# Kernel tuning notes

Measured on AMD Instinct MI355X. Metric: run time of the kernel, lower is better.

## Reference

```python
import jax, jax.numpy as jnp
import numpy as np

D_MODEL = 768
N_HEADS = 12
D_K = D_MODEL // N_HEADS


def setup_inputs() -> dict:
    key = jax.random.key(0)
    ks = jax.random.split(key, 9)
    s = 1.0 / np.sqrt(D_MODEL)
    return {
        "x": jax.random.normal(ks[0], (2, 2048, D_MODEL), dtype=jnp.float32),
        "w_q": jax.random.normal(ks[1], (D_MODEL, D_MODEL), dtype=jnp.float32) * s,
        "b_q": jax.random.normal(ks[2], (D_MODEL,), dtype=jnp.float32) * 0.02,
        "w_k": jax.random.normal(ks[3], (D_MODEL, D_MODEL), dtype=jnp.float32) * s,
        "b_k": jax.random.normal(ks[4], (D_MODEL,), dtype=jnp.float32) * 0.02,
        "w_v": jax.random.normal(ks[5], (D_MODEL, D_MODEL), dtype=jnp.float32) * s,
        "b_v": jax.random.normal(ks[6], (D_MODEL,), dtype=jnp.float32) * 0.02,
        "w_o": jax.random.normal(ks[7], (D_MODEL, D_MODEL), dtype=jnp.float32) * s,
        "b_o": jax.random.normal(ks[8], (D_MODEL,), dtype=jnp.float32) * 0.02,
    }


def reference(x, w_q, b_q, w_k, b_k, w_v, b_v, w_o, b_o):
    B, S, _ = x.shape
    # nn.Linear: y = x @ W^T + b
    def proj(w, b):
        y = jnp.einsum("bsd,ed->bse", x, w) + b
        # [B, S, D] -> [B, H, S, d_k]
        return y.reshape(B, S, N_HEADS, D_K).transpose(0, 2, 1, 3)

    q = proj(w_q, b_q)
    k = proj(w_k, b_k)
    v = proj(w_v, b_v)

    scale = 1.0 / np.sqrt(D_K).astype(np.float32)
    scores = jnp.einsum("bhqd,bhkd->bhqk", q, k) * scale  # [B,H,S,S]
    attn = jax.nn.softmax(scores, axis=-1)
    ctx = jnp.einsum("bhqk,bhkd->bhqd", attn, v)  # [B,H,S,d_k]
    ctx = ctx.transpose(0, 2, 1, 3).reshape(B, S, D_MODEL)
    out = jnp.einsum("bsd,ed->bse", ctx, w_o) + b_o
    return out
```

## Files before the change

### kernel.cpp

```cpp
#include <hip/hip_runtime.h>
#include <hip/hip_bf16.h>

#define B_   2
#define S_   2048
#define D_   768
#define H_   12
#define DK_  64
#define R_   (B_*S_)
#define LOG2E_OVER8 0.18033688011112042f

typedef __attribute__((ext_vector_type(8))) short short8;
typedef __attribute__((ext_vector_type(4))) float f32x4;

__device__ __forceinline__ short f2b(float f) {
  union { float f; unsigned u; } x; x.f = f;
  unsigned r = x.u + 0x7fffu + ((x.u >> 16) & 1u);
  return (short)(r >> 16);
}

__device__ __forceinline__ unsigned cvt_pk_bf16(float lo, float hi) {
  unsigned r;
  asm("v_cvt_pk_bf16_f32 %0, %1, %2" : "=v"(r) : "v"(lo), "v"(hi));
  return r;
}

__device__ __forceinline__ void gl_lds16(const short* g, short* l) {
  __builtin_amdgcn_global_load_lds(
      (const __attribute__((address_space(1))) void*)g,
      (__attribute__((address_space(3))) void*)l, 16, 0, 0);
}

__global__ void cvt_kernel(const float* __restrict__ x,
                           const float* __restrict__ wq, const float* __restrict__ wk,
                           const float* __restrict__ wv, const float* __restrict__ wo,
                           short* __restrict__ xb, short* __restrict__ wb) {
  const int XQ = R_ * D_ / 4;
  const int WQ = D_ * D_ / 4;
  int idx = blockIdx.x * blockDim.x + threadIdx.x;
  const float* src; short* dst; int off;
  if (idx < XQ) { src = x; dst = xb; off = idx; }
  else {
    int wi = idx - XQ; int w = wi / WQ; off = wi - w * WQ;
    if      (w == 0) { src = wq; dst = wb; }
    else if (w == 1) { src = wk; dst = wb + D_*D_; }
    else if (w == 2) { src = wv; dst = wb + 2*D_*D_; }
    else             { src = wo; dst = wb + 3*D_*D_; }
  }
  float4 v = ((const float4*)src)[off];
  short4 o;
  o.x = f2b(v.x); o.y = f2b(v.y); o.z = f2b(v.z); o.w = f2b(v.w);
  ((short4*)dst)[off] = o;
}

__launch_bounds__(256)
__global__ void qkv_gemm_kernel(const short* __restrict__ xb, const short* __restrict__ wb,
                                const float* __restrict__ bq, const float* __restrict__ bk,
                                const float* __restrict__ bv,
                                short* __restrict__ Qw, short* __restrict__ Kw,
                                short* __restrict__ VTw) {
  __shared__ short As[2][128 * 32];
  __shared__ short Bs[2][128 * 32];
  const int which = blockIdx.z;
  const short* W = wb + which * (D_ * D_);
  const float* bias = (which == 0) ? bq : (which == 1) ? bk : bv;
  const int n0 = blockIdx.x * 128, m0 = blockIdx.y * 128;
  const int t = threadIdx.x, l = t & 63, w = t >> 6;
  const int wr = w >> 1, wc = w & 1;

  f32x4 acc[4][4] = {};
  const int srow = t >> 2, sseg = (t & 3) * 8;

#define GSTAGE(buf, k0) do { \
    gl_lds16(xb + (m0 + srow) * D_ + (k0) + sseg,      &As[buf][t * 8]); \
    gl_lds16(xb + (m0 + 64 + srow) * D_ + (k0) + sseg, &As[buf][(t + 256) * 8]); \
    gl_lds16(W  + (n0 + srow) * D_ + (k0) + sseg,      &Bs[buf][t * 8]); \
    gl_lds16(W  + (n0 + 64 + srow) * D_ + (k0) + sseg, &Bs[buf][(t + 256) * 8]); \
  } while (0)

  GSTAGE(0, 0);
  __syncthreads();
  int cur = 0;
  for (int k0 = 0; k0 < D_; k0 += 32) {
    if (k0 + 32 < D_) GSTAGE(cur ^ 1, k0 + 32);
    short8 a[4], b[4];
#pragma unroll
    for (int i = 0; i < 4; i++)
      a[i] = *(const short8*)&As[cur][(wr * 64 + i * 16 + (l & 15)) * 32 + (l >> 4) * 8];
#pragma unroll
    for (int i = 0; i < 4; i++)
      b[i] = *(const short8*)&Bs[cur][(wc * 64 + i * 16 + (l & 15)) * 32 + (l >> 4) * 8];
#pragma unroll
    for (int i = 0; i < 4; i++)
#pragma unroll
      for (int j = 0; j < 4; j++)
        acc[i][j] = __builtin_amdgcn_mfma_f32_16x16x32_bf16(a[i], b[j], acc[i][j], 0, 0, 0);
    __syncthreads();
    cur ^= 1;
  }
#undef GSTAGE

#pragma unroll
  for (int i = 0; i < 4; i++) {
#pragma unroll
    for (int j2 = 0; j2 < 4; j2++) {
      int mm = m0 + wr * 64 + i * 16 + (l >> 4) * 4 + j2;
      int bidx = mm >> 11, s = mm & 2047;
#pragma unroll
      for (int nj = 0; nj < 4; nj++) {
        int e = n0 + wc * 64 + nj * 16 + (l & 15);
        float val = acc[i][nj][j2] + bias[e];
        int h = e >> 6, dk = e & 63;
        int bh = bidx * H_ + h;
        if (which == 0)      Qw[(bh * S_ + s) * DK_ + dk] = f2b(val * LOG2E_OVER8);
        else if (which == 1) Kw[(bh * S_ + s) * DK_ + dk] = f2b(val);
        else                 VTw[(bh * DK_ + dk) * S_ + s] = f2b(val);
      }
    }
  }
}

#define KVB   32
#define SHALF 1024
__launch_bounds__(256, 3)
__global__ void attn_kernel(const short* __restrict__ Qw, const short* __restrict__ Kw,
                            const short* __restrict__ VTw, short* __restrict__ ctx) {
  __shared__ short Ksh[2][2][KVB * DK_];
  __shared__ short Vsh[2][2][KVB * DK_];

  const int t = threadIdx.x, l = t & 63, w = t >> 6;
  const int s = w >> 1, qh = w & 1;
  const int L = blockIdx.y * 32 + blockIdx.x;
  const int xcd = L & 7, idx = L >> 3;
  const int bh = xcd * 3 + (idx >> 5);
  const int qblk = idx & 31;
  const int q0 = qblk * 64 + qh * 32;
  const int bq = bh / H_, h = bh - bq * H_;
  const short* Qh = Qw + bh * S_ * DK_;
  const short* Kh = Kw + (bh * S_ + s * SHALF) * DK_;
  const short* Vh = VTw + bh * DK_ * S_ + s * SHALF;

  const int tt = t & 127;
  const int kr0 = tt >> 3, kc0 = tt & 7;
  const int koff0 = kr0 * DK_ + ((kc0 ^ (kr0 & 7)) << 3);
  const int vc8 = (tt & 7) ^ ((tt >> 3) & 7);
  const int vr0 = 2 * (tt >> 3) + (vc8 >> 2);
  const int voff0 = vr0 * S_ + ((vc8 & 3) << 3);

#define STAGE(buf, kt) do { \
    gl_lds16(Kh + (kt) * DK_ + koff0,        &Ksh[s][buf][tt * 8]); \
    gl_lds16(Kh + (kt) * DK_ + koff0 + 1024, &Ksh[s][buf][tt * 8 + 1024]); \
    gl_lds16(Vh + (kt) + voff0,              &Vsh[s][buf][tt * 8]); \
    gl_lds16(Vh + (kt) + voff0 + 32 * S_,    &Vsh[s][buf][tt * 8 + 1024]); \
  } while (0)

  short8 qf[2][2];
#pragma unroll
  for (int mi = 0; mi < 2; mi++)
#pragma unroll
    for (int ks = 0; ks < 2; ks++)
      qf[mi][ks] = *(const short8*)&Qh[(q0 + 16 * mi + (l & 15)) * DK_ + ks * 32 + (l >> 4) * 8];

  f32x4 acc_o[2][4] = {};
  float l_run[2] = {0.f, 0.f};

  STAGE(0, 0);
  __syncthreads();
  int cur = 0;

  for (int kt = 0; kt < SHALF; kt += KVB) {
    if (kt + KVB < SHALF) STAGE(cur ^ 1, kt + KVB);

    f32x4 acc_s[2][2] = {};
    __builtin_amdgcn_s_setprio(1);
#pragma unroll
    for (int ni = 0; ni < 2; ni++) {
      int r = (l & 15) + 16 * ni;
#pragma unroll
      for (int ks = 0; ks < 2; ks++) {
        int cc = (l >> 4) + 4 * ks;
        short8 kf = *(const short8*)&Ksh[s][cur][r * DK_ + ((cc ^ (r & 7)) << 3)];
        acc_s[0][ni] = __builtin_amdgcn_mfma_f32_16x16x32_bf16(kf, qf[0][ks], acc_s[0][ni], 0, 0, 0);
        acc_s[1][ni] = __builtin_amdgcn_mfma_f32_16x16x32_bf16(kf, qf[1][ks], acc_s[1][ni], 0, 0, 0);
      }
    }
    __builtin_amdgcn_s_setprio(0);

#pragma unroll
    for (int mi = 0; mi < 2; mi++) {
      float sum = 0.f;
#pragma unroll
      for (int ni = 0; ni < 2; ni++)
#pragma unroll
        for (int j = 0; j < 4; j++) {
          float p = __builtin_amdgcn_exp2f(acc_s[mi][ni][j]);
          acc_s[mi][ni][j] = p;
          sum += p;
        }
      l_run[mi] += sum;
    }

    union PK { unsigned u[4]; short8 v; } pa0, pa1;
    pa0.u[0] = cvt_pk_bf16(acc_s[0][0][0], acc_s[0][0][1]);
    pa0.u[1] = cvt_pk_bf16(acc_s[0][0][2], acc_s[0][0][3]);
    pa0.u[2] = cvt_pk_bf16(acc_s[0][1][0], acc_s[0][1][1]);
    pa0.u[3] = cvt_pk_bf16(acc_s[0][1][2], acc_s[0][1][3]);
    pa1.u[0] = cvt_pk_bf16(acc_s[1][0][0], acc_s[1][0][1]);
    pa1.u[1] = cvt_pk_bf16(acc_s[1][0][2], acc_s[1][0][3]);
    pa1.u[2] = cvt_pk_bf16(acc_s[1][1][0], acc_s[1][1][1]);
    pa1.u[3] = cvt_pk_bf16(acc_s[1][1][2], acc_s[1][1][3]);

    __builtin_amdgcn_s_setprio(1);
    {
      const int cc = l >> 4;
      union V8 { short4 h[2]; short8 v; };
#pragma unroll
      for (int nd = 0; nd < 4; nd++) {
        int vr = (l & 15) + 16 * nd, rp = vr >> 1;
        int ph0 = (((vr & 1) << 2) | (cc >> 1)) ^ (rp & 7);
        int ph1 = (((vr & 1) << 2) | (2 + (cc >> 1))) ^ (rp & 7);
        V8 vf;
        vf.h[0] = *(const short4*)&Vsh[s][cur][rp * 64 + ph0 * 8 + (cc & 1) * 4];
        vf.h[1] = *(const short4*)&Vsh[s][cur][rp * 64 + ph1 * 8 + (cc & 1) * 4];
        acc_o[0][nd] = __builtin_amdgcn_mfma_f32_16x16x32_bf16(pa0.v, vf.v, acc_o[0][nd], 0, 0, 0);
        acc_o[1][nd] = __builtin_amdgcn_mfma_f32_16x16x32_bf16(pa1.v, vf.v, acc_o[1][nd], 0, 0, 0);
      }
    }
    __builtin_amdgcn_s_setprio(0);

    __syncthreads();
    cur ^= 1;
  }

#pragma unroll
  for (int mi = 0; mi < 2; mi++) {
    l_run[mi] += __shfl_xor(l_run[mi], 16);
    l_run[mi] += __shfl_xor(l_run[mi], 32);
  }

  __syncthreads();
  float* Oshf = (float*)&Ksh[0][0][0];
  float* Lsh  = (float*)&Vsh[0][0][0];
  if (s == 1) {
#pragma unroll
    for (int mi = 0; mi < 2; mi++)
#pragma unroll
      for (int nd = 0; nd < 4; nd++)
#pragma unroll
        for (int j = 0; j < 4; j++)
          Oshf[qh * 2048 + (16 * mi + (l >> 4) * 4 + j) * 64 + (l & 15) + 16 * nd] = acc_o[mi][nd][j];
    if (l < 16) {
      Lsh[(qh * 2 + 0) * 16 + l] = l_run[0];
      Lsh[(qh * 2 + 1) * 16 + l] = l_run[1];
    }
  }
  __syncthreads();
  if (s == 0) {
#pragma unroll
    for (int mi = 0; mi < 2; mi++) {
#pragma unroll
      for (int j = 0; j < 4; j++) {
        int src = ((l >> 4) << 2) + j;
        float llo = __shfl(l_run[mi], src);
        float lhi = Lsh[(qh * 2 + mi) * 16 + src];
        float inv = 1.f / (llo + lhi);
        int srow = q0 + 16 * mi + src;
#pragma unroll
        for (int nd = 0; nd < 4; nd++) {
          float ohi = Oshf[qh * 2048 + (16 * mi + src) * 64 + (l & 15) + 16 * nd];
          float val = (acc_o[mi][nd][j] + ohi) * inv;
          ctx[(bq * S_ + srow) * D_ + h * DK_ + (l & 15) + 16 * nd] = f2b(val);
        }
      }
    }
  }
#undef STAGE
}

__launch_bounds__(256)
__global__ void oproj_kernel(const short* __restrict__ ctx, const short* __restrict__ Wo,
                             const float* __restrict__ bo, float* __restrict__ out) {
  __shared__ short As[2][128 * 32];
  __shared__ short Bs[2][128 * 32];
  const int n0 = blockIdx.x * 128, m0 = blockIdx.y * 128;
  const int t = threadIdx.x, l = t & 63, w = t >> 6;
  const int wr = w >> 1, wc = w & 1;

  f32x4 acc[4][4] = {};
  const int srow = t >> 2, sseg = (t & 3) * 8;

#define GSTAGE(buf, k0) do { \
    gl_lds16(ctx + (m0 + srow) * D_ + (k0) + sseg,      &As[buf][t * 8]); \
    gl_lds16(ctx + (m0 + 64 + srow) * D_ + (k0) + sseg, &As[buf][(t + 256) * 8]); \
    gl_lds16(Wo  + (n0 + srow) * D_ + (k0) + sseg,      &Bs[buf][t * 8]); \
    gl_lds16(Wo  + (n0 + 64 + srow) * D_ + (k0) + sseg, &Bs[buf][(t + 256) * 8]); \
  } while (0)

  GSTAGE(0, 0);
  __syncthreads();
  int cur = 0;
  for (int k0 = 0; k0 < D_; k0 += 32) {
    if (k0 + 32 < D_) GSTAGE(cur ^ 1, k0 + 32);
    short8 a[4], b[4];
#pragma unroll
    for (int i = 0; i < 4; i++)
      a[i] = *(const short8*)&As[cur][(wr * 64 + i * 16 + (l & 15)) * 32 + (l >> 4) * 8];
#pragma unroll
    for (int i = 0; i < 4; i++)
      b[i] = *(const short8*)&Bs[cur][(wc * 64 + i * 16 + (l & 15)) * 32 + (l >> 4) * 8];
#pragma unroll
    for (int i = 0; i < 4; i++)
#pragma unroll
      for (int j = 0; j < 4; j++)
        acc[i][j] = __builtin_amdgcn_mfma_f32_16x16x32_bf16(a[i], b[j], acc[i][j], 0, 0, 0);
    __syncthreads();
    cur ^= 1;
  }
#undef GSTAGE

#pragma unroll
  for (int i = 0; i < 4; i++) {
#pragma unroll
    for (int j2 = 0; j2 < 4; j2++) {
      int mm = m0 + wr * 64 + i * 16 + (l >> 4) * 4 + j2;
#pragma unroll
      for (int nj = 0; nj < 4; nj++) {
        int e = n0 + wc * 64 + nj * 16 + (l & 15);
        out[mm * D_ + e] = acc[i][nj][j2] + bo[e];
      }
    }
  }
}

extern "C" void kernel_launch(void* const* d_in, const int* in_sizes, int n_in,
                              void* d_out, int out_size, void* d_ws, size_t ws_size,
                              hipStream_t stream) {
  (void)in_sizes; (void)n_in; (void)out_size; (void)ws_size;
  const float* x  = (const float*)d_in[0];
  const float* wq = (const float*)d_in[1];
  const float* bq = (const float*)d_in[2];
  const float* wk = (const float*)d_in[3];
  const float* bk = (const float*)d_in[4];
  const float* wv = (const float*)d_in[5];
  const float* bv = (const float*)d_in[6];
  const float* wo = (const float*)d_in[7];
  const float* bo = (const float*)d_in[8];
  float* out = (float*)d_out;

  short* xb  = (short*)d_ws;
  short* wb  = xb + R_ * D_;
  short* Qw  = wb + 4 * D_ * D_;
  short* Kw  = Qw + R_ * D_;
  short* VTw = Kw + R_ * D_;
  short* ctx = VTw + R_ * D_;

  cvt_kernel<<<5376, 256, 0, stream>>>(x, wq, wk, wv, wo, xb, wb);
  qkv_gemm_kernel<<<dim3(6, 32, 3), 256, 0, stream>>>(xb, wb, bq, bk, bv, Qw, Kw, VTw);
  attn_kernel<<<dim3(32, 24), 256, 0, stream>>>(Qw, Kw, VTw, ctx);
  oproj_kernel<<<dim3(6, 32), 256, 0, stream>>>(ctx, wb + 3 * D_ * D_, bo, out);
}
```

Baseline: 97.40 us.

## Shrink attention blocks to one wave per KV half and drop block barriers

The attention kernel now runs with 128 threads per block (two waves, one per KV half) over a 64x24 grid, so each wave stages and consumes its own K/V tiles in shared memory. Each wave issues its own loads and waits on them with an s_waitcnt vmcnt(8)/vmcnt(0) pattern instead of a block-wide __syncthreads each iteration. The goal is to remove barrier stalls and give the scheduler more independent blocks. The cost is loss of K/V sharing between the two query halves, which doubles K/V global traffic, and reliance on per-wave waitcnt for LDS visibility. The occupancy hint from launch bounds is also removed.

```diff
diff --git a/kernel.cpp b/kernel.cpp
--- a/kernel.cpp
+++ b/kernel.cpp
@@ -121,36 +121,35 @@
 
 #define KVB   32
 #define SHALF 1024
-__launch_bounds__(256, 3)
+__launch_bounds__(128)
 __global__ void attn_kernel(const short* __restrict__ Qw, const short* __restrict__ Kw,
                             const short* __restrict__ VTw, short* __restrict__ ctx) {
   __shared__ short Ksh[2][2][KVB * DK_];
   __shared__ short Vsh[2][2][KVB * DK_];
 
   const int t = threadIdx.x, l = t & 63, w = t >> 6;
-  const int s = w >> 1, qh = w & 1;
-  const int L = blockIdx.y * 32 + blockIdx.x;
+  const int L = blockIdx.y * 64 + blockIdx.x;
   const int xcd = L & 7, idx = L >> 3;
-  const int bh = xcd * 3 + (idx >> 5);
-  const int qblk = idx & 31;
-  const int q0 = qblk * 64 + qh * 32;
+  const int bh = xcd * 3 + (idx >> 6);
+  const int q0 = (idx & 63) * 32;
   const int bq = bh / H_, h = bh - bq * H_;
   const short* Qh = Qw + bh * S_ * DK_;
-  const short* Kh = Kw + (bh * S_ + s * SHALF) * DK_;
-  const short* Vh = VTw + bh * DK_ * S_ + s * SHALF;
-
-  const int tt = t & 127;
-  const int kr0 = tt >> 3, kc0 = tt & 7;
-  const int koff0 = kr0 * DK_ + ((kc0 ^ (kr0 & 7)) << 3);
-  const int vc8 = (tt & 7) ^ ((tt >> 3) & 7);
-  const int vr0 = 2 * (tt >> 3) + (vc8 >> 2);
+  const short* Kh = Kw + (bh * S_ + w * SHALF) * DK_;
+  const short* Vh = VTw + bh * DK_ * S_ + w * SHALF;
+
+  const int r0 = l >> 3, c0 = l & 7;
+  const int koff0 = r0 * DK_ + ((c0 ^ r0) << 3);
+  const int vc8 = c0 ^ r0;
+  const int vr0 = 2 * r0 + (vc8 >> 2);
   const int voff0 = vr0 * S_ + ((vc8 & 3) << 3);
 
 #define STAGE(buf, kt) do { \
-    gl_lds16(Kh + (kt) * DK_ + koff0,        &Ksh[s][buf][tt * 8]); \
-    gl_lds16(Kh + (kt) * DK_ + koff0 + 1024, &Ksh[s][buf][tt * 8 + 1024]); \
-    gl_lds16(Vh + (kt) + voff0,              &Vsh[s][buf][tt * 8]); \
-    gl_lds16(Vh + (kt) + voff0 + 32 * S_,    &Vsh[s][buf][tt * 8 + 1024]); \
+    _Pragma("unroll") \
+    for (int j = 0; j < 4; j++) \
+      gl_lds16(Kh + (kt) * DK_ + koff0 + 8 * j * DK_, &Ksh[w][buf][(l + 64 * j) * 8]); \
+    _Pragma("unroll") \
+    for (int j = 0; j < 4; j++) \
+      gl_lds16(Vh + (kt) + voff0 + 16 * S_ * j,       &Vsh[w][buf][(l + 64 * j) * 8]); \
   } while (0)
 
   short8 qf[2][2];
@@ -164,11 +163,16 @@
   float l_run[2] = {0.f, 0.f};
 
   STAGE(0, 0);
-  __syncthreads();
   int cur = 0;
 
   for (int kt = 0; kt < SHALF; kt += KVB) {
-    if (kt + KVB < SHALF) STAGE(cur ^ 1, kt + KVB);
+    if (kt + KVB < SHALF) {
+      STAGE(cur ^ 1, kt + KVB);
+      asm volatile("s_waitcnt vmcnt(8)" ::: "memory");
+    } else {
+      asm volatile("s_waitcnt vmcnt(0)" ::: "memory");
+    }
+    __builtin_amdgcn_sched_barrier(0);
 
     f32x4 acc_s[2][2] = {};
     __builtin_amdgcn_s_setprio(1);
@@ -178,7 +182,7 @@
 #pragma unroll
       for (int ks = 0; ks < 2; ks++) {
         int cc = (l >> 4) + 4 * ks;
-        short8 kf = *(const short8*)&Ksh[s][cur][r * DK_ + ((cc ^ (r & 7)) << 3)];
+        short8 kf = *(const short8*)&Ksh[w][cur][r * DK_ + ((cc ^ (r & 7)) << 3)];
         acc_s[0][ni] = __builtin_amdgcn_mfma_f32_16x16x32_bf16(kf, qf[0][ks], acc_s[0][ni], 0, 0, 0);
         acc_s[1][ni] = __builtin_amdgcn_mfma_f32_16x16x32_bf16(kf, qf[1][ks], acc_s[1][ni], 0, 0, 0);
       }
@@ -219,15 +223,14 @@
         int ph0 = (((vr & 1) << 2) | (cc >> 1)) ^ (rp & 7);
         int ph1 = (((vr & 1) << 2) | (2 + (cc >> 1))) ^ (rp & 7);
         V8 vf;
-        vf.h[0] = *(const short4*)&Vsh[s][cur][rp * 64 + ph0 * 8 + (cc & 1) * 4];
-        vf.h[1] = *(const short4*)&Vsh[s][cur][rp * 64 + ph1 * 8 + (cc & 1) * 4];
+        vf.h[0] = *(const short4*)&Vsh[w][cur][rp * 64 + ph0 * 8 + (cc & 1) * 4];
+        vf.h[1] = *(const short4*)&Vsh[w][cur][rp * 64 + ph1 * 8 + (cc & 1) * 4];
         acc_o[0][nd] = __builtin_amdgcn_mfma_f32_16x16x32_bf16(pa0.v, vf.v, acc_o[0][nd], 0, 0, 0);
         acc_o[1][nd] = __builtin_amdgcn_mfma_f32_16x16x32_bf16(pa1.v, vf.v, acc_o[1][nd], 0, 0, 0);
       }
     }
     __builtin_amdgcn_s_setprio(0);
 
-    __syncthreads();
     cur ^= 1;
   }
 
@@ -240,33 +243,33 @@
   __syncthreads();
   float* Oshf = (float*)&Ksh[0][0][0];
   float* Lsh  = (float*)&Vsh[0][0][0];
-  if (s == 1) {
+  if (w == 1) {
 #pragma unroll
     for (int mi = 0; mi < 2; mi++)
 #pragma unroll
       for (int nd = 0; nd < 4; nd++)
 #pragma unroll
         for (int j = 0; j < 4; j++)
-          Oshf[qh * 2048 + (16 * mi + (l >> 4) * 4 + j) * 64 + (l & 15) + 16 * nd] = acc_o[mi][nd][j];
+          Oshf[(16 * mi + (l >> 4) * 4 + j) * 64 + (l & 15) + 16 * nd] = acc_o[mi][nd][j];
     if (l < 16) {
-      Lsh[(qh * 2 + 0) * 16 + l] = l_run[0];
-      Lsh[(qh * 2 + 1) * 16 + l] = l_run[1];
+      Lsh[l]      = l_run[0];
+      Lsh[16 + l] = l_run[1];
     }
   }
   __syncthreads();
-  if (s == 0) {
+  if (w == 0) {
 #pragma unroll
     for (int mi = 0; mi < 2; mi++) {
 #pragma unroll
       for (int j = 0; j < 4; j++) {
         int src = ((l >> 4) << 2) + j;
         float llo = __shfl(l_run[mi], src);
-        float lhi = Lsh[(qh * 2 + mi) * 16 + src];
+        float lhi = Lsh[mi * 16 + src];
         float inv = 1.f / (llo + lhi);
         int srow = q0 + 16 * mi + src;
 #pragma unroll
         for (int nd = 0; nd < 4; nd++) {
-          float ohi = Oshf[qh * 2048 + (16 * mi + src) * 64 + (l & 15) + 16 * nd];
+          float ohi = Oshf[(16 * mi + src) * 64 + (l & 15) + 16 * nd];
           float val = (acc_o[mi][nd][j] + ohi) * inv;
           ctx[(bq * S_ + srow) * D_ + h * DK_ + (l & 15) + 16 * nd] = f2b(val);
         }
@@ -355,6 +358,6 @@
 
   cvt_kernel<<<5376, 256, 0, stream>>>(x, wq, wk, wv, wo, xb, wb);
   qkv_gemm_kernel<<<dim3(6, 32, 3), 256, 0, stream>>>(xb, wb, bq, bk, bv, Qw, Kw, VTw);
-  attn_kernel<<<dim3(32, 24), 256, 0, stream>>>(Qw, Kw, VTw, ctx);
+  attn_kernel<<<dim3(64, 24), 128, 0, stream>>>(Qw, Kw, VTw, ctx);
   oproj_kernel<<<dim3(6, 32), 256, 0, stream>>>(ctx, wb + 3 * D_ * D_, bo, out);
 }
```

New measurement: 126.4 us. +29.8%, slower.
